# Performance work log

Measured on AMD Instinct MI355X. Metric: run time of the kernel, lower is better.

## Reference

```python
import jax, jax.numpy as jnp
import numpy as np

EMBED_DIM = 512
NUM_HEADS = 8
HEAD_DIM = EMBED_DIM // NUM_HEADS
B, N, M = 4, 4096, 4096


def setup_inputs() -> dict:
    key = jax.random.key(0)
    ks = jax.random.split(key, 16)
    s = 0.02
    inp = {
        "query": jax.random.normal(ks[0], (B, N, EMBED_DIM), jnp.float32),
        "key": jax.random.normal(ks[1], (B, M, EMBED_DIM), jnp.float32),
        "value": jax.random.normal(ks[2], (B, M, EMBED_DIM), jnp.float32),
        # Linear weights stored as (in, out) so y = x @ W + b (== torch x @ W.T + b)
        "Wq": jax.random.normal(ks[3], (EMBED_DIM, EMBED_DIM), jnp.float32) * s,
        "bq": jnp.zeros((EMBED_DIM,), jnp.float32),
        "Wk": jax.random.normal(ks[4], (EMBED_DIM, EMBED_DIM), jnp.float32) * s,
        "bk": jnp.zeros((EMBED_DIM,), jnp.float32),
        "Wv": jax.random.normal(ks[5], (EMBED_DIM, EMBED_DIM), jnp.float32) * s,
        "bv": jnp.zeros((EMBED_DIM,), jnp.float32),
        # rank expansion MLP acts per-head on head_dim
        "W1": jax.random.normal(ks[6], (HEAD_DIM, HEAD_DIM * 2), jnp.float32) * s,
        "b1": jnp.zeros((HEAD_DIM * 2,), jnp.float32),
        "W2": jax.random.normal(ks[7], (HEAD_DIM * 2, HEAD_DIM), jnp.float32) * s,
        "b2": jnp.zeros((HEAD_DIM,), jnp.float32),
        "Wo": jax.random.normal(ks[8], (EMBED_DIM, EMBED_DIM), jnp.float32) * s,
        "bo": jnp.zeros((EMBED_DIM,), jnp.float32),
    }
    return inp


def reference(query, key, value, Wq, bq, Wk, bk, Wv, bv, W1, b1, W2, b2, Wo, bo):
    b, n, _ = query.shape
    m = key.shape[1]
    H, D = NUM_HEADS, HEAD_DIM
    # ELU+1 feature maps on projected q, k
    q = jax.nn.elu(query @ Wq + bq) + 1.0           # [B,N,E]
    k = jax.nn.elu(key @ Wk + bk) + 1.0             # [B,M,E]
    v = value @ Wv + bv                              # [B,M,E]
    q = q.reshape(b, n, H, D)
    k = k.reshape(b, m, H, D)
    v = v.reshape(b, m, H, D)
    # rank expansion MLP on keys (per head_dim), exact GELU as nn.GELU default
    k_aug = jax.nn.gelu(k @ W1 + b1, approximate=False) @ W2 + b2
    k_aug = jax.nn.elu(k_aug) + 1.0                  # [B,M,H,D]
    # inputs already fp32 (torch .float() casts are identity here)
    k_scaled = k_aug / m                             # normalize over context len
    kv_context = jnp.einsum('bmhd,bmhe->bhde', k_scaled, v)   # [B,H,D,D]
    out = jnp.einsum('bnhd,bhde->bnhe', q, kv_context)        # [B,N,H,D]
    k_sum = k_scaled.sum(axis=1)                      # [B,H,D]
    denom = jnp.einsum('bnhd,bhd->bnh', q, k_sum)     # [B,N,H]
    out = out / jnp.clip(denom, 1e-6, None)[..., None]
    out = jnp.clip(jnp.nan_to_num(out, nan=0.0, posinf=65000.0, neginf=-65000.0),
                   -65000.0, 65000.0)
    out = out.reshape(b, n, H * D)
    return out @ Wo + bo
```

## Files before the change

kernel.cpp:

```cpp
#include <hip/hip_runtime.h>
#include <cmath>

#define DEV __device__ __forceinline__

typedef __bf16 bf16x8 __attribute__((ext_vector_type(8)));
typedef float f32x4 __attribute__((ext_vector_type(4)));
typedef unsigned int u32;
typedef unsigned short u16;

DEV u16 f2bf(float f) {
  union { float f; u32 u; } v;
  v.f = f;
  u32 u = v.u;
  u += 0x7fffu + ((u >> 16) & 1u);
  return (u16)(u >> 16);
}
DEV float bf2f(u16 h) {
  union { u32 u; float f; } v;
  v.u = ((u32)h) << 16;
  return v.f;
}

DEV void async16(const u16* g, u16* l) {
  __builtin_amdgcn_global_load_lds((const __attribute__((address_space(1))) u32*)g,
                                   (__attribute__((address_space(3))) u32*)l, 16, 0, 0);
}

enum { ACT_ID = 0, ACT_ELU1 = 1, ACT_GELU = 2, ACT_ELU1S = 3 };
enum { AM_ROW = 0, AM_BH = 1 };
enum { OM_ROW = 0, OM_VT = 1, OM_KAT = 2 };

DEV float apply_act(int ACT, float v, float scale) {
  if (ACT == ACT_ELU1)  return (v > 0.f) ? (v + 1.f) : __expf(v);
  if (ACT == ACT_GELU)  return 0.5f * v * (1.f + erff(v * 0.7071067811865475f));
  if (ACT == ACT_ELU1S) return ((v > 0.f) ? (v + 1.f) : __expf(v)) * scale;
  return v;
}

template <int BM, int BN, int K, int WR, int WC, int ACT, int OBF16, int AMODE, int OMODE>
__global__ __launch_bounds__(256)
void gemm_bf16(const u16* __restrict__ A, const u16* __restrict__ Bt,
               const float* __restrict__ bias, void* __restrict__ Yv,
               int NC, float scale)
{
  constexpr int AI = BM / 64;
  constexpr int BI = BN / 64;
  __shared__ u16 As[BM * 32];
  __shared__ u16 Bs[BN * 32];
  static_assert(WR * WC == 4, "4 waves");

  const int tid = threadIdx.x;
  const int wv = tid >> 6, lane = tid & 63;
  const int wr = wv / WC, wc = wv % WC;
  const int lrow = lane & 15, lq = lane >> 4;
  const int c0 = blockIdx.x * BN;

  long arow_base;
  int arstride;
  long r0 = 0;
  int bh = 0, m0 = 0;
  if (AMODE == AM_ROW) {
    r0 = (long)blockIdx.y * BM;
    arow_base = r0 * K;
    arstride = K;
  } else {
    bh = blockIdx.y >> 4;
    m0 = (blockIdx.y & 15) * BM;
    const int b = bh >> 3, h = bh & 7;
    arow_base = (long)b * 4194304 + (long)h * 128 + (long)m0 * 1024;
    arstride = 1024;
  }

  f32x4 acc[4][4] = {};

  for (int kt = 0; kt < K; kt += 32) {
#pragma unroll
    for (int i = 0; i < AI; ++i) {
      const int s = (wv * AI + i) * 64 + lane;
      async16(A + arow_base + (long)(s >> 2) * arstride + kt + (s & 3) * 8,
              &As[(wv * AI + i) * 512]);
    }
#pragma unroll
    for (int i = 0; i < BI; ++i) {
      const int s = (wv * BI + i) * 64 + lane;
      async16(Bt + ((long)c0 + (s >> 2)) * K + kt + (s & 3) * 8,
              &Bs[(wv * BI + i) * 512]);
    }
    __syncthreads();
    bf16x8 af[4], bfr[4];
#pragma unroll
    for (int i = 0; i < 4; ++i)
      af[i] = *(const bf16x8*)&As[(wr * 64 + i * 16 + lrow) * 32 + lq * 8];
#pragma unroll
    for (int j = 0; j < 4; ++j)
      bfr[j] = *(const bf16x8*)&Bs[(wc * 64 + j * 16 + lrow) * 32 + lq * 8];
#pragma unroll
    for (int i = 0; i < 4; ++i)
#pragma unroll
      for (int j = 0; j < 4; ++j)
        acc[i][j] = __builtin_amdgcn_mfma_f32_16x16x32_bf16(af[i], bfr[j], acc[i][j], 0, 0, 0);
    __syncthreads();
  }

  float* Yf = (float*)Yv;
  u16* Yh = (u16*)Yv;
#pragma unroll
  for (int i = 0; i < 4; ++i) {
#pragma unroll
    for (int j = 0; j < 4; ++j) {
      const int col = c0 + wc * 64 + j * 16 + lrow;
      const float bv = bias[col];
      float o[4];
#pragma unroll
      for (int p = 0; p < 4; ++p) o[p] = apply_act(ACT, acc[i][j][p] + bv, scale);

      if (OMODE == OM_ROW) {
#pragma unroll
        for (int p = 0; p < 4; ++p) {
          const long row = r0 + wr * 64 + i * 16 + lq * 4 + p;
          const long yi = row * NC + col;
          if (OBF16) Yh[yi] = f2bf(o[p]);
          else       Yf[yi] = o[p];
        }
      } else if (OMODE == OM_VT) {
        const int b = (int)(r0 >> 12);
        const int m = (int)(r0 & 4095) + wr * 64 + i * 16 + lq * 4;
        const int h = col >> 6, e = col & 63;
        ushort4 w;
        w.x = f2bf(o[0]); w.y = f2bf(o[1]); w.z = f2bf(o[2]); w.w = f2bf(o[3]);
        *(ushort4*)(Yh + (((long)b * 8 + h) * 64 + e) * 4096 + m) = w;
      } else {
        const int m = m0 + wr * 64 + i * 16 + lq * 4;
        ushort4 w;
        w.x = f2bf(o[0]); w.y = f2bf(o[1]); w.z = f2bf(o[2]); w.w = f2bf(o[3]);
        *(ushort4*)(Yh + ((long)bh * 64 + col) * 4096 + m) = w;
      }
    }
  }
}

__global__ __launch_bounds__(256)
void cvt_qkv(const float* __restrict__ s0, const float* __restrict__ s1,
             const float* __restrict__ s2, u16* __restrict__ d0,
             u16* __restrict__ d1, u16* __restrict__ d2)
{
  const float* s = blockIdx.y == 0 ? s0 : blockIdx.y == 1 ? s1 : s2;
  u16* d = blockIdx.y == 0 ? d0 : blockIdx.y == 1 ? d1 : d2;
  const long i = ((long)blockIdx.x * 256 + threadIdx.x) * 8;
  float4 a = *(const float4*)(s + i);
  float4 b = *(const float4*)(s + i + 4);
  ushort4 w0, w1;
  w0.x = f2bf(a.x); w0.y = f2bf(a.y); w0.z = f2bf(a.z); w0.w = f2bf(a.w);
  w1.x = f2bf(b.x); w1.y = f2bf(b.y); w1.z = f2bf(b.z); w1.w = f2bf(b.w);
  *(ushort4*)(d + i) = w0;
  *(ushort4*)(d + i + 4) = w1;
}

struct TArgs {
  const float* src[6];
  u16* dst[6];
  int K[6];
  int N[6];
};
__global__ __launch_bounds__(256)
void transpose_w(TArgs a)
{
  const int m = blockIdx.z;
  const int K = a.K[m], N = a.N[m];
  const int kt = blockIdx.y * 64, nt = blockIdx.x * 64;
  if (kt >= K || nt >= N) return;
  const float* src = a.src[m];
  u16* dst = a.dst[m];
  __shared__ u16 t[64][72];
  const int tx = threadIdx.x & 15, ty = threadIdx.x >> 4;
#pragma unroll
  for (int rr = 0; rr < 64; rr += 16) {
    const int k = kt + ty + rr;
    float4 v = *(const float4*)(src + (long)k * N + nt + tx * 4);
    t[tx * 4 + 0][ty + rr] = f2bf(v.x);
    t[tx * 4 + 1][ty + rr] = f2bf(v.y);
    t[tx * 4 + 2][ty + rr] = f2bf(v.z);
    t[tx * 4 + 3][ty + rr] = f2bf(v.w);
  }
  __syncthreads();
#pragma unroll
  for (int it = 0; it < 2; ++it) {
    const int s = threadIdx.x + it * 256;
    const int r = s >> 3, c = (s & 7) * 8;
    ushort4 u0 = *(ushort4*)&t[r][c];
    ushort4 u1 = *(ushort4*)&t[r][c + 4];
    *(ushort4*)(dst + (long)(nt + r) * K + kt + c) = u0;
    *(ushort4*)(dst + (long)(nt + r) * K + kt + c + 4) = u1;
  }
}

__global__ __launch_bounds__(256)
void kv_gemm(const u16* __restrict__ kaT, const u16* __restrict__ vT,
             float* __restrict__ kvp, float* __restrict__ ksp)
{
  const int sp = blockIdx.x;
  const int bh = blockIdx.y;
  __shared__ u16 SB[16384];
  u16* As = SB;
  u16* Bs = SB + 8192;
  const int tid = threadIdx.x, wv = tid >> 6, lane = tid & 63;
  const int lrow = lane & 15, lq = lane >> 4;
  f32x4 acc[4][4] = {};
  f32x4 accs[4] = {};
  bf16x8 ones;
#pragma unroll
  for (int z = 0; z < 8; ++z) ones[z] = (__bf16)1.0f;
  const long base = (long)bh * 64 * 4096;

  for (int ph = 0; ph < 4; ++ph) {
    const int m0 = sp * 512 + ph * 128;
#pragma unroll
    for (int i = 0; i < 4; ++i) {
      const int s = (wv * 4 + i) * 64 + lane;
      const int chunk = s >> 8, row = (s >> 2) & 63, part = s & 3;
      const long g = base + (long)row * 4096 + m0 + chunk * 32 + part * 8;
      async16(kaT + g, &As[(wv * 4 + i) * 512]);
      async16(vT + g, &Bs[(wv * 4 + i) * 512]);
    }
    __syncthreads();
    bf16x8 af[4], bfr[4];
#pragma unroll
    for (int i = 0; i < 4; ++i)
      af[i] = *(const bf16x8*)&As[wv * 2048 + (i * 16 + lrow) * 32 + lq * 8];
#pragma unroll
    for (int j = 0; j < 4; ++j)
      bfr[j] = *(const bf16x8*)&Bs[wv * 2048 + (j * 16 + lrow) * 32 + lq * 8];
#pragma unroll
    for (int i = 0; i < 4; ++i) {
#pragma unroll
      for (int j = 0; j < 4; ++j)
        acc[i][j] = __builtin_amdgcn_mfma_f32_16x16x32_bf16(af[i], bfr[j], acc[i][j], 0, 0, 0);
      accs[i] = __builtin_amdgcn_mfma_f32_16x16x32_bf16(af[i], ones, accs[i], 0, 0, 0);
    }
    __syncthreads();
  }

  float* red = (float*)SB;
  float* ksr = red + 64 * 68;
  for (int w = 0; w < 4; ++w) {
    __syncthreads();
    if (wv == w) {
#pragma unroll
      for (int i = 0; i < 4; ++i) {
#pragma unroll
        for (int j = 0; j < 4; ++j) {
          const int e = j * 16 + lrow, d0 = i * 16 + lq * 4;
          float* p = &red[e * 68 + d0];
          if (w == 0) { p[0] = acc[i][j][0]; p[1] = acc[i][j][1]; p[2] = acc[i][j][2]; p[3] = acc[i][j][3]; }
          else        { p[0] += acc[i][j][0]; p[1] += acc[i][j][1]; p[2] += acc[i][j][2]; p[3] += acc[i][j][3]; }
        }
        if (lrow == 0) {
          const int d0 = i * 16 + lq * 4;
#pragma unroll
          for (int p2 = 0; p2 < 4; ++p2) {
            if (w == 0) ksr[d0 + p2] = accs[i][p2];
            else        ksr[d0 + p2] += accs[i][p2];
          }
        }
      }
    }
  }
  __syncthreads();
  float* kvo = kvp + ((long)sp * 32 + bh) * 4096;
  for (int s = tid; s < 4096; s += 256) kvo[s] = red[(s >> 6) * 68 + (s & 63)];
  if (tid < 64) ksp[(sp * 32 + bh) * 64 + tid] = ksr[tid];
}

__global__ __launch_bounds__(256)
void kv_reduce(const float* __restrict__ kvp, const float* __restrict__ ksp,
               u16* __restrict__ kvT, u16* __restrict__ ksumT)
{
  const int bh = blockIdx.x;
  const int t = threadIdx.x;
  for (int s = t; s < 4096; s += 256) {
    float v = 0.f;
#pragma unroll
    for (int sp = 0; sp < 8; ++sp) v += kvp[((long)sp * 32 + bh) * 4096 + s];
    kvT[(long)bh * 4096 + s] = f2bf(v);
  }
  if (t < 64) {
    float v = 0.f;
#pragma unroll
    for (int sp = 0; sp < 8; ++sp) v += ksp[(sp * 32 + bh) * 64 + t];
    ksumT[bh * 64 + t] = f2bf(v);
  }
}

__global__ __launch_bounds__(256)
void attn_mfma(const u16* __restrict__ q, const u16* __restrict__ kvT,
               const u16* __restrict__ ksumT, u16* __restrict__ attn)
{
  __shared__ u16 SB[17408];
  const int tid = threadIdx.x, wv = tid >> 6, lane = tid & 63;
  const int lrow = lane & 15, lq = lane >> 4;
  const int n0 = blockIdx.x * 256;
  const int bh = blockIdx.y, b = bh >> 3, h = bh & 7;
  u16* As = SB;

#pragma unroll
  for (int half = 0; half < 2; ++half)
#pragma unroll
    for (int i = 0; i < 4; ++i) {
      const int s = (wv * 4 + i) * 64 + lane;
      async16(q + ((long)(b * 4096 + n0 + (s >> 2))) * 512 + h * 64 + half * 32 + (s & 3) * 8,
              &As[half * 8192 + (wv * 4 + i) * 512]);
    }
  bf16x8 bfr[2][4], ks[2];
#pragma unroll
  for (int half = 0; half < 2; ++half) {
#pragma unroll
    for (int j = 0; j < 4; ++j)
      bfr[half][j] = *(const bf16x8*)(kvT + ((long)bh * 64 + j * 16 + lrow) * 64 + half * 32 + lq * 8);
    ks[half] = *(const bf16x8*)(ksumT + bh * 64 + half * 32 + lq * 8);
  }
  __syncthreads();

  f32x4 acc[4][4] = {};
  f32x4 accd[4] = {};
#pragma unroll
  for (int half = 0; half < 2; ++half) {
    bf16x8 af[4];
#pragma unroll
    for (int i = 0; i < 4; ++i)
      af[i] = *(const bf16x8*)&As[half * 8192 + (wv * 64 + i * 16 + lrow) * 32 + lq * 8];
#pragma unroll
    for (int i = 0; i < 4; ++i) {
#pragma unroll
      for (int j = 0; j < 4; ++j)
        acc[i][j] = __builtin_amdgcn_mfma_f32_16x16x32_bf16(af[i], bfr[half][j], acc[i][j], 0, 0, 0);
      accd[i] = __builtin_amdgcn_mfma_f32_16x16x32_bf16(af[i], ks[half], accd[i], 0, 0, 0);
    }
  }
  __syncthreads();

  u16* LT = SB;
#pragma unroll
  for (int i = 0; i < 4; ++i) {
    float dinv[4];
#pragma unroll
    for (int p = 0; p < 4; ++p) dinv[p] = 1.f / fmaxf(accd[i][p], 1e-6f);
#pragma unroll
    for (int j = 0; j < 4; ++j) {
      const int e = j * 16 + lrow;
      const int nl0 = i * 16 + lq * 4;
      ushort4 w;
      float x0 = acc[i][j][0] * dinv[0], x1 = acc[i][j][1] * dinv[1];
      float x2 = acc[i][j][2] * dinv[2], x3 = acc[i][j][3] * dinv[3];
      if (!(x0 == x0)) x0 = 0.f;
      if (!(x1 == x1)) x1 = 0.f;
      if (!(x2 == x2)) x2 = 0.f;
      if (!(x3 == x3)) x3 = 0.f;
      w.x = f2bf(fminf(65000.f, fmaxf(-65000.f, x0)));
      w.y = f2bf(fminf(65000.f, fmaxf(-65000.f, x1)));
      w.z = f2bf(fminf(65000.f, fmaxf(-65000.f, x2)));
      w.w = f2bf(fminf(65000.f, fmaxf(-65000.f, x3)));
      *(ushort4*)&LT[wv * 4352 + e * 68 + nl0] = w;
    }
  }
  __syncthreads();
#pragma unroll
  for (int it = 0; it < 8; ++it) {
    const int c = it * 256 + tid;
    const int n = c & 255, ec = c >> 8;
    const int wr2 = n >> 6, nl = n & 63;
    ushort4 w0, w1;
    w0.x = LT[wr2 * 4352 + (ec * 8 + 0) * 68 + nl];
    w0.y = LT[wr2 * 4352 + (ec * 8 + 1) * 68 + nl];
    w0.z = LT[wr2 * 4352 + (ec * 8 + 2) * 68 + nl];
    w0.w = LT[wr2 * 4352 + (ec * 8 + 3) * 68 + nl];
    w1.x = LT[wr2 * 4352 + (ec * 8 + 4) * 68 + nl];
    w1.y = LT[wr2 * 4352 + (ec * 8 + 5) * 68 + nl];
    w1.z = LT[wr2 * 4352 + (ec * 8 + 6) * 68 + nl];
    w1.w = LT[wr2 * 4352 + (ec * 8 + 7) * 68 + nl];
    u16* dst = attn + ((long)(b * 4096 + n0 + n)) * 512 + h * 64 + ec * 8;
    *(ushort4*)dst = w0;
    *(ushort4*)(dst + 4) = w1;
  }
}

static constexpr long U = 8388608;

extern "C" void kernel_launch(void* const* d_in, const int* in_sizes, int n_in,
                              void* d_out, int out_size, void* d_ws, size_t ws_size,
                              hipStream_t stream)
{
  const float* query = (const float*)d_in[0];
  const float* key   = (const float*)d_in[1];
  const float* value = (const float*)d_in[2];
  const float* Wq = (const float*)d_in[3];
  const float* bq = (const float*)d_in[4];
  const float* Wk = (const float*)d_in[5];
  const float* bk = (const float*)d_in[6];
  const float* Wv = (const float*)d_in[7];
  const float* bv = (const float*)d_in[8];
  const float* W1 = (const float*)d_in[9];
  const float* b1 = (const float*)d_in[10];
  const float* W2 = (const float*)d_in[11];
  const float* b2 = (const float*)d_in[12];
  const float* Wo = (const float*)d_in[13];
  const float* bo = (const float*)d_in[14];

  u16* wsh = (u16*)d_ws;
  u16* qbf  = wsh;
  u16* kbf  = wsh + U;
  u16* vbf  = wsh + 2 * U;
  u16* qact = wsh + 3 * U;
  u16* kact = wsh + 4 * U;
  u16* vT   = wsh + 5 * U;
  u16* hid  = qbf;
  u16* kaT  = vbf;
  u16* attn = kact;

  float* fp  = (float*)(wsh + 6 * U);
  float* kvp = fp;
  float* ksp = fp + 1048576;
  u16* kvTg   = (u16*)(fp + 1064960);
  u16* ksumTg = kvTg + 131072;
  u16* wtb = ksumTg + 2048;
  u16* WqT = wtb;
  u16* WkT = wtb + 262144;
  u16* WvT = wtb + 524288;
  u16* WoT = wtb + 786432;
  u16* W1T = wtb + 1048576;
  u16* W2T = wtb + 1056768;

  dim3 blk(256);
  const float invM = 1.f / 4096.f;

  TArgs ta;
  ta.src[0] = Wq; ta.dst[0] = WqT; ta.K[0] = 512; ta.N[0] = 512;
  ta.src[1] = Wk; ta.dst[1] = WkT; ta.K[1] = 512; ta.N[1] = 512;
  ta.src[2] = Wv; ta.dst[2] = WvT; ta.K[2] = 512; ta.N[2] = 512;
  ta.src[3] = Wo; ta.dst[3] = WoT; ta.K[3] = 512; ta.N[3] = 512;
  ta.src[4] = W1; ta.dst[4] = W1T; ta.K[4] = 64;  ta.N[4] = 128;
  ta.src[5] = W2; ta.dst[5] = W2T; ta.K[5] = 128; ta.N[5] = 64;
  transpose_w<<<dim3(8, 8, 6), blk, 0, stream>>>(ta);

  cvt_qkv<<<dim3(4096, 3), blk, 0, stream>>>(query, key, value, qbf, kbf, vbf);

  gemm_bf16<128,128,512,2,2,ACT_ELU1,1,AM_ROW,OM_ROW><<<dim3(4,128), blk, 0, stream>>>(qbf, WqT, bq, qact, 512, 1.f);
  gemm_bf16<128,128,512,2,2,ACT_ELU1,1,AM_ROW,OM_ROW><<<dim3(4,128), blk, 0, stream>>>(kbf, WkT, bk, kact, 512, 1.f);
  gemm_bf16<128,128,512,2,2,ACT_ID,  1,AM_ROW,OM_VT ><<<dim3(4,128), blk, 0, stream>>>(vbf, WvT, bv, vT,   512, 1.f);
  gemm_bf16<128,128,64,2,2,ACT_GELU,1,AM_ROW,OM_ROW><<<dim3(1,1024), blk, 0, stream>>>(kact, W1T, b1, hid, 128, 1.f);
  gemm_bf16<256,64,128,4,1,ACT_ELU1S,1,AM_BH,OM_KAT><<<dim3(1,512), blk, 0, stream>>>(hid, W2T, b2, kaT, 64, invM);
  kv_gemm<<<dim3(8,32), blk, 0, stream>>>(kaT, vT, kvp, ksp);
  kv_reduce<<<dim3(32), blk, 0, stream>>>(kvp, ksp, kvTg, ksumTg);
  attn_mfma<<<dim3(16,32), blk, 0, stream>>>(qact, kvTg, ksumTg, attn);
  gemm_bf16<128,128,512,2,2,ACT_ID,0,AM_ROW,OM_ROW><<<dim3(4,128), blk, 0, stream>>>(attn, WoT, bo, (float*)d_out, 512, 1.f);
}
```

Baseline: 296.6 us.

## Fuse fp32-to-bf16 conversion into projection GEMMs and fuse rank-expansion MLP

Removes the separate cvt_qkv pass: the projection GEMMs now load fp32 activations straight into swizzled LDS and convert to bf16 in registers. The two MLP GEMMs (W1+GELU, W2+ELU) become one kernel that keeps the hidden activations in LDS, so the hidden tensor no longer makes a round trip through global memory. kv_gemm is split over twice as many blocks along m to raise parallelism, and kv_reduce sums twice as many partials. In exchange the projection GEMMs read twice the A bytes into LDS and convert in the inner loop, and the fused MLP writes kaT with scalar strided stores.

```diff
diff --git a/kernel.cpp b/kernel.cpp
--- a/kernel.cpp
+++ b/kernel.cpp
@@ -15,20 +15,19 @@
   u += 0x7fffu + ((u >> 16) & 1u);
   return (u16)(u >> 16);
 }
-DEV float bf2f(u16 h) {
-  union { u32 u; float f; } v;
-  v.u = ((u32)h) << 16;
-  return v.f;
-}
-
-DEV void async16(const u16* g, u16* l) {
+DEV __bf16 bfbits(u16 b) {
+  union { u16 u; __bf16 h; } v;
+  v.u = b;
+  return v.h;
+}
+
+DEV void async16(const void* g, void* l) {
   __builtin_amdgcn_global_load_lds((const __attribute__((address_space(1))) u32*)g,
                                    (__attribute__((address_space(3))) u32*)l, 16, 0, 0);
 }
 
 enum { ACT_ID = 0, ACT_ELU1 = 1, ACT_GELU = 2, ACT_ELU1S = 3 };
-enum { AM_ROW = 0, AM_BH = 1 };
-enum { OM_ROW = 0, OM_VT = 1, OM_KAT = 2 };
+enum { OM_ROW = 0, OM_VT = 1 };
 
 DEV float apply_act(int ACT, float v, float scale) {
   if (ACT == ACT_ELU1)  return (v > 0.f) ? (v + 1.f) : __expf(v);
@@ -37,15 +36,16 @@
   return v;
 }
 
-template <int BM, int BN, int K, int WR, int WC, int ACT, int OBF16, int AMODE, int OMODE>
+template <int BM, int BN, int K, int WR, int WC, int ACT, int OBF16, int OMODE, int AFP32>
 __global__ __launch_bounds__(256)
-void gemm_bf16(const u16* __restrict__ A, const u16* __restrict__ Bt,
+void gemm_bf16(const void* __restrict__ Av, const u16* __restrict__ Bt,
                const float* __restrict__ bias, void* __restrict__ Yv,
                int NC, float scale)
 {
-  constexpr int AI = BM / 64;
+  constexpr int AI = AFP32 ? BM / 32 : BM / 64;
   constexpr int BI = BN / 64;
-  __shared__ u16 As[BM * 32];
+  constexpr int ABYTES = AFP32 ? BM * 128 : BM * 64;
+  __shared__ __align__(16) char AsRaw[ABYTES];
   __shared__ u16 Bs[BN * 32];
   static_assert(WR * WC == 4, "4 waves");
 
@@ -54,43 +54,53 @@
   const int wr = wv / WC, wc = wv % WC;
   const int lrow = lane & 15, lq = lane >> 4;
   const int c0 = blockIdx.x * BN;
-
-  long arow_base;
-  int arstride;
-  long r0 = 0;
-  int bh = 0, m0 = 0;
-  if (AMODE == AM_ROW) {
-    r0 = (long)blockIdx.y * BM;
-    arow_base = r0 * K;
-    arstride = K;
-  } else {
-    bh = blockIdx.y >> 4;
-    m0 = (blockIdx.y & 15) * BM;
-    const int b = bh >> 3, h = bh & 7;
-    arow_base = (long)b * 4194304 + (long)h * 128 + (long)m0 * 1024;
-    arstride = 1024;
-  }
+  const long r0 = (long)blockIdx.y * BM;
+  const float* Af = (const float*)Av;
+  const u16* Ah = (const u16*)Av;
 
   f32x4 acc[4][4] = {};
 
   for (int kt = 0; kt < K; kt += 32) {
-#pragma unroll
-    for (int i = 0; i < AI; ++i) {
-      const int s = (wv * AI + i) * 64 + lane;
-      async16(A + arow_base + (long)(s >> 2) * arstride + kt + (s & 3) * 8,
-              &As[(wv * AI + i) * 512]);
+    if (AFP32) {
+#pragma unroll
+      for (int i = 0; i < AI; ++i) {
+        const int s = (wv * AI + i) * 64 + lane;
+        const int row = s >> 3, p = s & 7;
+        const int gp = p ^ (row & 7);
+        async16(Af + (r0 + row) * K + kt + gp * 4, AsRaw + (wv * AI + i) * 1024);
+      }
+    } else {
+#pragma unroll
+      for (int i = 0; i < AI; ++i) {
+        const int s = (wv * AI + i) * 64 + lane;
+        async16(Ah + (r0 + (s >> 2)) * (long)K + kt + (s & 3) * 8,
+                AsRaw + (wv * AI + i) * 1024);
+      }
     }
 #pragma unroll
     for (int i = 0; i < BI; ++i) {
       const int s = (wv * BI + i) * 64 + lane;
       async16(Bt + ((long)c0 + (s >> 2)) * K + kt + (s & 3) * 8,
-              &Bs[(wv * BI + i) * 512]);
+              (char*)Bs + (wv * BI + i) * 1024);
     }
     __syncthreads();
     bf16x8 af[4], bfr[4];
 #pragma unroll
-    for (int i = 0; i < 4; ++i)
-      af[i] = *(const bf16x8*)&As[(wr * 64 + i * 16 + lrow) * 32 + lq * 8];
+    for (int i = 0; i < 4; ++i) {
+      const int r = wr * 64 + i * 16 + lrow;
+      if (AFP32) {
+        const float* Asf = (const float*)AsRaw;
+        const int r7 = r & 7, P0 = lq * 2;
+        float4 lo = *(const float4*)&Asf[r * 32 + (P0 ^ r7) * 4];
+        float4 hi = *(const float4*)&Asf[r * 32 + ((P0 + 1) ^ r7) * 4];
+        af[i][0] = bfbits(f2bf(lo.x)); af[i][1] = bfbits(f2bf(lo.y));
+        af[i][2] = bfbits(f2bf(lo.z)); af[i][3] = bfbits(f2bf(lo.w));
+        af[i][4] = bfbits(f2bf(hi.x)); af[i][5] = bfbits(f2bf(hi.y));
+        af[i][6] = bfbits(f2bf(hi.z)); af[i][7] = bfbits(f2bf(hi.w));
+      } else {
+        af[i] = *(const bf16x8*)((const u16*)AsRaw + r * 32 + lq * 8);
+      }
+    }
 #pragma unroll
     for (int j = 0; j < 4; ++j)
       bfr[j] = *(const bf16x8*)&Bs[(wc * 64 + j * 16 + lrow) * 32 + lq * 8];
@@ -122,38 +132,16 @@
           if (OBF16) Yh[yi] = f2bf(o[p]);
           else       Yf[yi] = o[p];
         }
-      } else if (OMODE == OM_VT) {
+      } else {
         const int b = (int)(r0 >> 12);
         const int m = (int)(r0 & 4095) + wr * 64 + i * 16 + lq * 4;
         const int h = col >> 6, e = col & 63;
         ushort4 w;
         w.x = f2bf(o[0]); w.y = f2bf(o[1]); w.z = f2bf(o[2]); w.w = f2bf(o[3]);
         *(ushort4*)(Yh + (((long)b * 8 + h) * 64 + e) * 4096 + m) = w;
-      } else {
-        const int m = m0 + wr * 64 + i * 16 + lq * 4;
-        ushort4 w;
-        w.x = f2bf(o[0]); w.y = f2bf(o[1]); w.z = f2bf(o[2]); w.w = f2bf(o[3]);
-        *(ushort4*)(Yh + ((long)bh * 64 + col) * 4096 + m) = w;
       }
     }
   }
-}
-
-__global__ __launch_bounds__(256)
-void cvt_qkv(const float* __restrict__ s0, const float* __restrict__ s1,
-             const float* __restrict__ s2, u16* __restrict__ d0,
-             u16* __restrict__ d1, u16* __restrict__ d2)
-{
-  const float* s = blockIdx.y == 0 ? s0 : blockIdx.y == 1 ? s1 : s2;
-  u16* d = blockIdx.y == 0 ? d0 : blockIdx.y == 1 ? d1 : d2;
-  const long i = ((long)blockIdx.x * 256 + threadIdx.x) * 8;
-  float4 a = *(const float4*)(s + i);
-  float4 b = *(const float4*)(s + i + 4);
-  ushort4 w0, w1;
-  w0.x = f2bf(a.x); w0.y = f2bf(a.y); w0.z = f2bf(a.z); w0.w = f2bf(a.w);
-  w1.x = f2bf(b.x); w1.y = f2bf(b.y); w1.z = f2bf(b.z); w1.w = f2bf(b.w);
-  *(ushort4*)(d + i) = w0;
-  *(ushort4*)(d + i + 4) = w1;
 }
 
 struct TArgs {
@@ -191,6 +179,120 @@
     ushort4 u1 = *(ushort4*)&t[r][c + 4];
     *(ushort4*)(dst + (long)(nt + r) * K + kt + c) = u0;
     *(ushort4*)(dst + (long)(nt + r) * K + kt + c + 4) = u1;
+  }
+}
+
+__global__ __launch_bounds__(256)
+void mlp_fused(const u16* __restrict__ kact, const u16* __restrict__ W1T,
+               const u16* __restrict__ W2T, const float* __restrict__ b1,
+               const float* __restrict__ b2, u16* __restrict__ kaT, float invM)
+{
+  __shared__ __align__(16) u16 SB[27136];
+  u16* As  = SB;
+  u16* W1p = SB + 9216;
+  u16* W2p = SB + 18432;
+  u16* hid = SB;
+
+  const int tid = threadIdx.x, wv = tid >> 6, lane = tid & 63;
+  const int lrow = lane & 15, lq = lane >> 4;
+  const int bh = blockIdx.y, b = bh >> 3, h = bh & 7;
+  const int m0 = blockIdx.x * 128;
+  const long kbase = ((long)b * 4096 + m0) * 512 + h * 64;
+
+#pragma unroll
+  for (int i = 0; i < 4; ++i) {
+    const int c = i * 256 + tid;
+    const int row = c >> 3, p = c & 7;
+    uint4 v = *(const uint4*)(kact + kbase + (long)row * 512 + p * 8);
+    *(uint4*)&As[row * 72 + p * 8] = v;
+  }
+#pragma unroll
+  for (int i = 0; i < 4; ++i) {
+    const int c = i * 256 + tid;
+    const int row = c >> 3, p = c & 7;
+    uint4 v = *(const uint4*)(W1T + c * 8);
+    *(uint4*)&W1p[row * 72 + p * 8] = v;
+  }
+#pragma unroll
+  for (int i = 0; i < 4; ++i) {
+    const int c = i * 256 + tid;
+    const int row = c >> 4, p = c & 15;
+    uint4 v = *(const uint4*)(W2T + c * 8);
+    *(uint4*)&W2p[row * 136 + p * 8] = v;
+  }
+  __syncthreads();
+
+  const int c0 = (wv >> 1) * 64, mh0 = (wv & 1) * 64;
+  f32x4 acc1[4][4] = {};
+#pragma unroll
+  for (int kt = 0; kt < 2; ++kt) {
+    bf16x8 wa[4], kb[4];
+#pragma unroll
+    for (int i = 0; i < 4; ++i)
+      wa[i] = *(const bf16x8*)&W1p[(c0 + i * 16 + lrow) * 72 + kt * 32 + lq * 8];
+#pragma unroll
+    for (int j = 0; j < 4; ++j)
+      kb[j] = *(const bf16x8*)&As[(mh0 + j * 16 + lrow) * 72 + kt * 32 + lq * 8];
+#pragma unroll
+    for (int i = 0; i < 4; ++i)
+#pragma unroll
+      for (int j = 0; j < 4; ++j)
+        acc1[i][j] = __builtin_amdgcn_mfma_f32_16x16x32_bf16(wa[i], kb[j], acc1[i][j], 0, 0, 0);
+  }
+  __syncthreads();
+
+#pragma unroll
+  for (int i = 0; i < 4; ++i) {
+    const int cc = c0 + i * 16 + lq * 4;
+    float4 bv = *(const float4*)(b1 + cc);
+#pragma unroll
+    for (int j = 0; j < 4; ++j) {
+      const int m = mh0 + j * 16 + lrow;
+      float x0 = acc1[i][j][0] + bv.x, x1 = acc1[i][j][1] + bv.y;
+      float x2 = acc1[i][j][2] + bv.z, x3 = acc1[i][j][3] + bv.w;
+      ushort4 w;
+      w.x = f2bf(0.5f * x0 * (1.f + erff(x0 * 0.7071067811865475f)));
+      w.y = f2bf(0.5f * x1 * (1.f + erff(x1 * 0.7071067811865475f)));
+      w.z = f2bf(0.5f * x2 * (1.f + erff(x2 * 0.7071067811865475f)));
+      w.w = f2bf(0.5f * x3 * (1.f + erff(x3 * 0.7071067811865475f)));
+      *(ushort4*)&hid[m * 136 + cc] = w;
+    }
+  }
+  __syncthreads();
+
+  const int d0 = (wv >> 1) * 32, mh2 = (wv & 1) * 64;
+  f32x4 acc2[2][4] = {};
+#pragma unroll
+  for (int kt = 0; kt < 4; ++kt) {
+    bf16x8 wa[2], hb[4];
+#pragma unroll
+    for (int i = 0; i < 2; ++i)
+      wa[i] = *(const bf16x8*)&W2p[(d0 + i * 16 + lrow) * 136 + kt * 32 + lq * 8];
+#pragma unroll
+    for (int j = 0; j < 4; ++j)
+      hb[j] = *(const bf16x8*)&hid[(mh2 + j * 16 + lrow) * 136 + kt * 32 + lq * 8];
+#pragma unroll
+    for (int i = 0; i < 2; ++i)
+#pragma unroll
+      for (int j = 0; j < 4; ++j)
+        acc2[i][j] = __builtin_amdgcn_mfma_f32_16x16x32_bf16(wa[i], hb[j], acc2[i][j], 0, 0, 0);
+  }
+
+#pragma unroll
+  for (int i = 0; i < 2; ++i) {
+    const int dd = d0 + i * 16 + lq * 4;
+    float4 bv = *(const float4*)(b2 + dd);
+    float bva[4] = {bv.x, bv.y, bv.z, bv.w};
+#pragma unroll
+    for (int j = 0; j < 4; ++j) {
+      const int m = m0 + mh2 + j * 16 + lrow;
+#pragma unroll
+      for (int p = 0; p < 4; ++p) {
+        float v = acc2[i][j][p] + bva[p];
+        v = ((v > 0.f) ? (v + 1.f) : __expf(v)) * invM;
+        kaT[((long)bh * 64 + dd + p) * 4096 + m] = f2bf(v);
+      }
+    }
   }
 }
 
@@ -212,8 +314,8 @@
   for (int z = 0; z < 8; ++z) ones[z] = (__bf16)1.0f;
   const long base = (long)bh * 64 * 4096;
 
-  for (int ph = 0; ph < 4; ++ph) {
-    const int m0 = sp * 512 + ph * 128;
+  for (int ph = 0; ph < 2; ++ph) {
+    const int m0 = sp * 256 + ph * 128;
 #pragma unroll
     for (int i = 0; i < 4; ++i) {
       const int s = (wv * 4 + i) * 64 + lane;
@@ -249,17 +351,17 @@
       for (int i = 0; i < 4; ++i) {
 #pragma unroll
         for (int j = 0; j < 4; ++j) {
-          const int e = j * 16 + lrow, d0 = i * 16 + lq * 4;
-          float* p = &red[e * 68 + d0];
+          const int e = j * 16 + lrow, dd = i * 16 + lq * 4;
+          float* p = &red[e * 68 + dd];
           if (w == 0) { p[0] = acc[i][j][0]; p[1] = acc[i][j][1]; p[2] = acc[i][j][2]; p[3] = acc[i][j][3]; }
           else        { p[0] += acc[i][j][0]; p[1] += acc[i][j][1]; p[2] += acc[i][j][2]; p[3] += acc[i][j][3]; }
         }
         if (lrow == 0) {
-          const int d0 = i * 16 + lq * 4;
+          const int dd = i * 16 + lq * 4;
 #pragma unroll
           for (int p2 = 0; p2 < 4; ++p2) {
-            if (w == 0) ksr[d0 + p2] = accs[i][p2];
-            else        ksr[d0 + p2] += accs[i][p2];
+            if (w == 0) ksr[dd + p2] = accs[i][p2];
+            else        ksr[dd + p2] += accs[i][p2];
           }
         }
       }
@@ -280,13 +382,13 @@
   for (int s = t; s < 4096; s += 256) {
     float v = 0.f;
 #pragma unroll
-    for (int sp = 0; sp < 8; ++sp) v += kvp[((long)sp * 32 + bh) * 4096 + s];
+    for (int sp = 0; sp < 16; ++sp) v += kvp[((long)sp * 32 + bh) * 4096 + s];
     kvT[(long)bh * 4096 + s] = f2bf(v);
   }
   if (t < 64) {
     float v = 0.f;
 #pragma unroll
-    for (int sp = 0; sp < 8; ++sp) v += ksp[(sp * 32 + bh) * 64 + t];
+    for (int sp = 0; sp < 16; ++sp) v += ksp[(sp * 32 + bh) * 64 + t];
     ksumT[bh * 64 + t] = f2bf(v);
   }
 }
@@ -406,20 +508,16 @@
   const float* bo = (const float*)d_in[14];
 
   u16* wsh = (u16*)d_ws;
-  u16* qbf  = wsh;
-  u16* kbf  = wsh + U;
-  u16* vbf  = wsh + 2 * U;
-  u16* qact = wsh + 3 * U;
-  u16* kact = wsh + 4 * U;
-  u16* vT   = wsh + 5 * U;
-  u16* hid  = qbf;
-  u16* kaT  = vbf;
-  u16* attn = kact;
-
-  float* fp  = (float*)(wsh + 6 * U);
+  u16* qact = wsh;
+  u16* kact = wsh + U;
+  u16* vT   = wsh + 2 * U;
+  u16* kaT  = wsh + 3 * U;
+  u16* attn = wsh + 4 * U;
+
+  float* fp  = (float*)(wsh + 5 * U);
   float* kvp = fp;
-  float* ksp = fp + 1048576;
-  u16* kvTg   = (u16*)(fp + 1064960);
+  float* ksp = fp + 2097152;
+  u16* kvTg   = (u16*)(fp + 2129920);
   u16* ksumTg = kvTg + 131072;
   u16* wtb = ksumTg + 2048;
   u16* WqT = wtb;
@@ -441,15 +539,12 @@
   ta.src[5] = W2; ta.dst[5] = W2T; ta.K[5] = 128; ta.N[5] = 64;
   transpose_w<<<dim3(8, 8, 6), blk, 0, stream>>>(ta);
 
-  cvt_qkv<<<dim3(4096, 3), blk, 0, stream>>>(query, key, value, qbf, kbf, vbf);
-
-  gemm_bf16<128,128,512,2,2,ACT_ELU1,1,AM_ROW,OM_ROW><<<dim3(4,128), blk, 0, stream>>>(qbf, WqT, bq, qact, 512, 1.f);
-  gemm_bf16<128,128,512,2,2,ACT_ELU1,1,AM_ROW,OM_ROW><<<dim3(4,128), blk, 0, stream>>>(kbf, WkT, bk, kact, 512, 1.f);
-  gemm_bf16<128,128,512,2,2,ACT_ID,  1,AM_ROW,OM_VT ><<<dim3(4,128), blk, 0, stream>>>(vbf, WvT, bv, vT,   512, 1.f);
-  gemm_bf16<128,128,64,2,2,ACT_GELU,1,AM_ROW,OM_ROW><<<dim3(1,1024), blk, 0, stream>>>(kact, W1T, b1, hid, 128, 1.f);
-  gemm_bf16<256,64,128,4,1,ACT_ELU1S,1,AM_BH,OM_KAT><<<dim3(1,512), blk, 0, stream>>>(hid, W2T, b2, kaT, 64, invM);
-  kv_gemm<<<dim3(8,32), blk, 0, stream>>>(kaT, vT, kvp, ksp);
+  gemm_bf16<128,128,512,2,2,ACT_ELU1,1,OM_ROW,1><<<dim3(4,128), blk, 0, stream>>>(query, WqT, bq, qact, 512, 1.f);
+  gemm_bf16<128,128,512,2,2,ACT_ELU1,1,OM_ROW,1><<<dim3(4,128), blk, 0, stream>>>(key,   WkT, bk, kact, 512, 1.f);
+  gemm_bf16<128,128,512,2,2,ACT_ID,  1,OM_VT, 1><<<dim3(4,128), blk, 0, stream>>>(value, WvT, bv, vT,   512, 1.f);
+  mlp_fused<<<dim3(32,32), blk, 0, stream>>>(kact, W1T, W2T, b1, b2, kaT, invM);
+  kv_gemm<<<dim3(16,32), blk, 0, stream>>>(kaT, vT, kvp, ksp);
   kv_reduce<<<dim3(32), blk, 0, stream>>>(kvp, ksp, kvTg, ksumTg);
   attn_mfma<<<dim3(16,32), blk, 0, stream>>>(qact, kvTg, ksumTg, attn);
-  gemm_bf16<128,128,512,2,2,ACT_ID,0,AM_ROW,OM_ROW><<<dim3(4,128), blk, 0, stream>>>(attn, WoT, bo, (float*)d_out, 512, 1.f);
-}
+  gemm_bf16<128,128,512,2,2,ACT_ID,0,OM_ROW,0><<<dim3(4,128), blk, 0, stream>>>(attn, WoT, bo, (float*)d_out, 512, 1.f);
+}
```

Measured after the change: 295.3 us. Within noise of the previous version (-0.4%).
